# Performance work log

Measured on AMD Instinct MI355X. Metric: run time of the kernel, lower is better.

Reference implementation:

```python
import jax, jax.numpy as jnp
import numpy as np

FILTER_SZ = 5  # matches init_kwargs filter_sz


def setup_inputs() -> dict:
    key = jax.random.key(0)
    image = jax.random.normal(key, (16, 3, 512, 512), dtype=jnp.float32)
    return {"image": image}


def reference(image):
    # scipy.ndimage.median_filter with default mode='reflect' ((d c b a | a b c d)),
    # which corresponds to jnp.pad mode='symmetric'.
    k = FILTER_SZ
    pad = k // 2
    B, C, H, W = image.shape
    padded = jnp.pad(image, ((0, 0), (0, 0), (pad, pad), (pad, pad)), mode="symmetric")
    # Gather all k*k shifted views: [B, C, H, W, k*k]. Fixed small loop over the
    # window offsets (k*k = 25), fully vectorized over batch/channel/spatial dims.
    patches = jnp.stack(
        [padded[:, :, i:i + H, j:j + W] for i in range(k) for j in range(k)],
        axis=-1,
    )
    # Order statistic: median of the k*k window per pixel.
    return jnp.median(patches, axis=-1)
```

## Files before the change

kernel.cpp:

```cpp
#include <hip/hip_runtime.h>


typedef _Float16 h2 __attribute__((ext_vector_type(2)));

static __device__ __forceinline__ h2 h2min(h2 a, h2 b) { return __builtin_elementwise_min(a, b); }
static __device__ __forceinline__ h2 h2max(h2 a, h2 b) { return __builtin_elementwise_max(a, b); }

static __device__ __forceinline__ h2 pack2(float a, float b) {
    return __builtin_bit_cast(h2, __builtin_amdgcn_cvt_pkrtz(a, b));
}

#define CAS(a, b) do { h2 _mn = h2min((a), (b)); (b) = h2max((a), (b)); (a) = _mn; } while (0)

static __device__ __forceinline__ void sort5(h2 &e0, h2 &e1, h2 &e2, h2 &e3, h2 &e4) {
    CAS(e0, e1); CAS(e3, e4); CAS(e2, e4); CAS(e2, e3); CAS(e0, e3);
    CAS(e0, e2); CAS(e1, e4); CAS(e1, e3); CAS(e1, e2);
}

#define MINMAX8(w0, w1, w2, w3, w4, w5, w6, w7) do {      \
    CAS(w0, w1); CAS(w2, w3); CAS(w4, w5); CAS(w6, w7);   \
    CAS(w0, w2); CAS(w4, w6); CAS(w0, w4);                \
    CAS(w1, w3); CAS(w5, w7); CAS(w3, w7); } while (0)

#define MINMAX5(v0, v1, v2, v3, v4) do {                  \
    CAS(v0, v1); CAS(v2, v3); CAS(v0, v2); CAS(v1, v3);   \
    CAS(v0, v4); CAS(v3, v4); } while (0)

static __device__ __forceinline__ h2 sel7of13(h2 c0, h2 c1, h2 c2, h2 c3, h2 c4, h2 c5, h2 c6,
                                              h2 c7, h2 c8, h2 c9, h2 c10, h2 c11, h2 c12) {
    MINMAX8(c0, c1, c2, c3, c4, c5, c6, c7); c0 = c8;  c7 = c9;
    MINMAX8(c0, c1, c2, c3, c4, c5, c6, c7); c0 = c10; c7 = c11;
    MINMAX8(c0, c1, c2, c3, c4, c5, c6, c7); c0 = c12;
    MINMAX5(c0, c1, c2, c3, c4); c0 = c5; c4 = c6;
    MINMAX5(c0, c1, c2, c3, c4);
    CAS(c1, c2); CAS(c2, c3); CAS(c1, c2);
    return c2;
}

static __device__ __forceinline__ int refl(int v, int n) {
    v = (v < 0) ? (-v - 1) : v;
    return (v >= n) ? (2 * n - 1 - v) : v;
}

static __device__ __forceinline__ void load_sorted_row(h2 (&dst)[5], const float* __restrict__ rp,
                                                       const int (&xo)[6]) {
    float f0 = rp[xo[0]], f1 = rp[xo[1]], f2 = rp[xo[2]],
          f3 = rp[xo[3]], f4 = rp[xo[4]], f5 = rp[xo[5]];
    dst[0] = pack2(f0, f1);
    dst[1] = pack2(f1, f2);
    dst[2] = pack2(f2, f3);
    dst[3] = pack2(f3, f4);
    dst[4] = pack2(f4, f5);
    sort5(dst[0], dst[1], dst[2], dst[3], dst[4]);
}

constexpr int W = 512, H = 512, R = 8;

__global__ __launch_bounds__(256) void median5x5_kernel(const float* __restrict__ in,
                                                        float* __restrict__ out) {
    const int tx = blockIdx.x * 64 + threadIdx.x;
    const int x0 = 2 * tx;
    const int ystrip = blockIdx.y * 4 + threadIdx.y;
    const int y0 = ystrip * R;
    const size_t plane = (size_t)blockIdx.z * ((size_t)H * W);
    const float* __restrict__ p = in + plane;
    float* __restrict__ q = out + plane;

    int xo[6];
    #pragma unroll
    for (int d = 0; d < 6; ++d) xo[d] = refl(x0 - 2 + d, W);

    h2 rows[5][5];

    #pragma unroll
    for (int k = 0; k < 4; ++k)
        load_sorted_row(rows[k], p + (size_t)refl(y0 - 2 + k, H) * W, xo);

    #pragma unroll
    for (int t = 0; t < R; ++t) {
        load_sorted_row(rows[(4 + t) % 5], p + (size_t)refl(y0 + 2 + t, H) * W, xo);

        h2 (&s0)[5] = rows[(t + 0) % 5];
        h2 (&s1)[5] = rows[(t + 1) % 5];
        h2 (&s2)[5] = rows[(t + 2) % 5];
        h2 (&s3)[5] = rows[(t + 3) % 5];
        h2 (&s4)[5] = rows[(t + 4) % 5];

        h2 a0=s0[0], a1=s1[0], a2=s2[0], a3=s3[0], a4=s4[0]; sort5(a0,a1,a2,a3,a4);
        h2 b0=s0[1], b1=s1[1], b2=s2[1], b3=s3[1], b4=s4[1]; sort5(b0,b1,b2,b3,b4);
        h2 c0=s0[2], c1=s1[2], c2=s2[2], c3=s3[2], c4=s4[2]; sort5(c0,c1,c2,c3,c4);
        h2 d0=s0[3], d1=s1[3], d2=s2[3], d3=s3[3], d4=s4[3]; sort5(d0,d1,d2,d3,d4);
        h2 e0=s0[4], e1=s1[4], e2=s2[4], e3=s3[4], e4=s4[4]; sort5(e0,e1,e2,e3,e4);
        (void)a0; (void)a1; (void)a2; (void)b0; (void)b1; (void)c0; (void)c4;
        (void)d3; (void)d4; (void)e2; (void)e3; (void)e4;

        h2 med = sel7of13(d0, e0, c1, d1, e1, b2, c2, d2, a3, b3, c3, a4, b4);

        float2 o;
        o.x = (float)med.x;
        o.y = (float)med.y;
        *reinterpret_cast<float2*>(q + (size_t)(y0 + t) * W + x0) = o;
    }
}

extern "C" void kernel_launch(void* const* d_in, const int* in_sizes, int n_in,
                              void* d_out, int out_size, void* d_ws, size_t ws_size,
                              hipStream_t stream) {
    const float* in = (const float*)d_in[0];
    float* out = (float*)d_out;
    dim3 block(64, 4, 1);
    dim3 grid(512 / (64 * 2), 512 / (4 * R), 16 * 3);
    hipLaunchKernelGGL(median5x5_kernel, grid, block, 0, stream, in, out);
}
```

Baseline: 124.9 us.

## Stage input tile with halo in LDS before median computation

Each block now cooperatively loads a 36x132 halo tile of the input plane into shared memory, with reflection applied during the load, and then synchronises. Threads read their row windows from LDS as float2 pairs instead of issuing six scalar global loads per row. This is meant to cut redundant global and L1 traffic, since neighbouring threads and strips overlap in the rows and columns they read. The cost is about 19 KB of LDS per block, a barrier, and a staging loop with an integer division for indexing.

Measured after the change: 136.1 us. 1.09x slower.

```diff
diff --git a/kernel.cpp b/kernel.cpp
--- a/kernel.cpp
+++ b/kernel.cpp
@@ -42,43 +42,58 @@
     return (v >= n) ? (2 * n - 1 - v) : v;
 }
 
-static __device__ __forceinline__ void load_sorted_row(h2 (&dst)[5], const float* __restrict__ rp,
-                                                       const int (&xo)[6]) {
-    float f0 = rp[xo[0]], f1 = rp[xo[1]], f2 = rp[xo[2]],
-          f3 = rp[xo[3]], f4 = rp[xo[4]], f5 = rp[xo[5]];
-    dst[0] = pack2(f0, f1);
-    dst[1] = pack2(f1, f2);
-    dst[2] = pack2(f2, f3);
-    dst[3] = pack2(f3, f4);
-    dst[4] = pack2(f4, f5);
+constexpr int W = 512, H = 512, R = 8;
+constexpr int TILE_W = 132;
+constexpr int TILE_H = 36;
+
+static __device__ __forceinline__ void row_from_lds(h2 (&dst)[5], const float* lp) {
+    const float2* rp = (const float2*)lp;
+    float2 u = rp[0], v = rp[1], w2 = rp[2];
+    dst[0] = pack2(u.x, u.y);
+    dst[1] = pack2(u.y, v.x);
+    dst[2] = pack2(v.x, v.y);
+    dst[3] = pack2(v.y, w2.x);
+    dst[4] = pack2(w2.x, w2.y);
     sort5(dst[0], dst[1], dst[2], dst[3], dst[4]);
 }
 
-constexpr int W = 512, H = 512, R = 8;
-
 __global__ __launch_bounds__(256) void median5x5_kernel(const float* __restrict__ in,
                                                         float* __restrict__ out) {
-    const int tx = blockIdx.x * 64 + threadIdx.x;
-    const int x0 = 2 * tx;
-    const int ystrip = blockIdx.y * 4 + threadIdx.y;
-    const int y0 = ystrip * R;
+    __shared__ float ld[TILE_H][TILE_W];
+
+    const int lx = threadIdx.x;
+    const int ty = threadIdx.y;
+    const int tid = ty * 64 + lx;
     const size_t plane = (size_t)blockIdx.z * ((size_t)H * W);
     const float* __restrict__ p = in + plane;
     float* __restrict__ q = out + plane;
 
-    int xo[6];
+    const int xbase = blockIdx.x * 128 - 2;
+    const int ybase = blockIdx.y * 32 - 2;
     #pragma unroll
-    for (int d = 0; d < 6; ++d) xo[d] = refl(x0 - 2 + d, W);
+    for (int e = 0; e < TILE_W * TILE_H; e += 256) {
+        int idx = e + tid;
+        if (idx < TILE_W * TILE_H) {
+            int r = idx / TILE_W;
+            int i = idx - r * TILE_W;
+            ld[r][i] = p[(size_t)refl(ybase + r, H) * W + refl(xbase + i, W)];
+        }
+    }
+    __syncthreads();
+
+    const int x0 = blockIdx.x * 128 + 2 * lx;
+    const int y0 = blockIdx.y * 32 + ty * R;
+    const int r0 = ty * R;
+    const float* lp = &ld[0][2 * lx];
 
     h2 rows[5][5];
-
     #pragma unroll
     for (int k = 0; k < 4; ++k)
-        load_sorted_row(rows[k], p + (size_t)refl(y0 - 2 + k, H) * W, xo);
+        row_from_lds(rows[k], lp + (r0 + k) * TILE_W);
 
     #pragma unroll
     for (int t = 0; t < R; ++t) {
-        load_sorted_row(rows[(4 + t) % 5], p + (size_t)refl(y0 + 2 + t, H) * W, xo);
+        row_from_lds(rows[(4 + t) % 5], lp + (r0 + t + 4) * TILE_W);
 
         h2 (&s0)[5] = rows[(t + 0) % 5];
         h2 (&s1)[5] = rows[(t + 1) % 5];
@@ -109,6 +124,6 @@
     const float* in = (const float*)d_in[0];
     float* out = (float*)d_out;
     dim3 block(64, 4, 1);
-    dim3 grid(512 / (64 * 2), 512 / (4 * R), 16 * 3);
+    dim3 grid(512 / 128, 512 / 32, 16 * 3);
     hipLaunchKernelGGL(median5x5_kernel, grid, block, 0, stream, in, out);
 }
```
